# Optimization experiments

Measured on AMD Instinct MI355X. Metric: run time of the kernel, lower is better.

The kernel has to match this reference:

```python
import jax, jax.numpy as jnp
import numpy as np

B, N, M, D = 4, 4096, 4096, 128


def setup_inputs() -> dict:
    key = jax.random.key(0)
    kk, kq, kv = jax.random.split(key, 3)
    return {
        "k": jax.random.normal(kk, (B, N, D), dtype=jnp.float32),
        "q": jax.random.normal(kq, (B, M, D), dtype=jnp.float32),
        "v": jax.random.normal(kv, (B, M, D), dtype=jnp.float32),
    }


def reference(k, q, v):
    # scores: [B, N, M] = k @ q^T
    scores = jnp.einsum("bnd,bmd->bnm", k, q)
    # Original uses nn.Softmax() with no dim; torch's legacy rule resolves
    # dim=0 for 3-D inputs, so softmax is over the batch axis, applied twice.
    w = jax.nn.softmax(jax.nn.softmax(scores, axis=0), axis=0)
    out = jnp.einsum("bnm,bmd->bnd", w, v)
    return out
```

## Files before the change

kernel.cpp:

```cpp
#include <hip/hip_runtime.h>
#include <hip/hip_bf16.h>

#define NB 4
#define NN 4096
#define MM 4096
#define DD 128
#define BN 32
#define BM 64
#define NCH 4
#define OUT_ELEMS ((size_t)NB * NN * DD)

using f32x4  = __attribute__((ext_vector_type(4))) float;
using bf16x8 = __attribute__((ext_vector_type(8))) short;

__device__ __forceinline__ float fast_exp2(float x) {
  return __builtin_amdgcn_exp2f(x);
}

__device__ __forceinline__ int rfl(int x) {
  return __builtin_amdgcn_readfirstlane(x);
}

__device__ __forceinline__ short f2bf(float x) {
  union { __hip_bfloat16 h; short s; } u;
  u.h = __float2bfloat16(x);
  return u.s;
}

__device__ __forceinline__ float bf2f(unsigned short s) {
  union { float f; unsigned u; } u;
  u.u = ((unsigned)s) << 16;
  return u.f;
}

__device__ __forceinline__ bf16x8 pack8(const float* __restrict__ p) {
  float4 a = *(const float4*)p;
  float4 b = *(const float4*)(p + 4);
  bf16x8 r;
  r[0] = f2bf(a.x); r[1] = f2bf(a.y); r[2] = f2bf(a.z); r[3] = f2bf(a.w);
  r[4] = f2bf(b.x); r[5] = f2bf(b.y); r[6] = f2bf(b.z); r[7] = f2bf(b.w);
  return r;
}

__global__ __launch_bounds__(256) void zero_out_kernel(float4* __restrict__ out) {
  out[(size_t)blockIdx.x * 256 + threadIdx.x] = (float4){0.f, 0.f, 0.f, 0.f};
}

__global__ __launch_bounds__(256) void prep_kernel(
    const float* __restrict__ k, const float* __restrict__ q, const float* __restrict__ v,
    unsigned short* __restrict__ kbt, unsigned short* __restrict__ qbt,
    unsigned short* __restrict__ vtt) {
  __shared__ unsigned short t[64][72];
  if (blockIdx.y < 2) {
    const float* src = blockIdx.y ? q : k;
    unsigned short* dst = blockIdx.y ? qbt : kbt;
    const int blk = blockIdx.x;
    const int b = blk >> 8, rf = blk & 255;
    const int kf = threadIdx.x >> 6, l = threadIdx.x & 63;
    const int lr = l & 15, hg = l >> 4;
    const float* s = src + ((size_t)(b * 4096 + rf * 16 + lr) * DD + kf * 32 + hg * 8);
    *(bf16x8*)(dst + (((size_t)((b * 256 + rf) * 4 + kf)) << 9) + (l << 3)) = pack8(s);
    return;
  }
  if (blockIdx.x >= 512) return;
  const int b = blockIdx.x >> 7;
  const int rem = blockIdx.x & 127;
  const int d0 = (rem >> 6) * 64, m0 = (rem & 63) * 64;
  const int r = threadIdx.x >> 2, c4 = threadIdx.x & 3;
  const float* src = v + ((size_t)b * MM + m0 + r) * DD + d0 + c4 * 16;
  for (int j = 0; j < 4; ++j) {
    float4 x = *(const float4*)(src + j * 4);
    int dl = c4 * 16 + j * 4;
    t[dl + 0][r] = (unsigned short)f2bf(x.x);
    t[dl + 1][r] = (unsigned short)f2bf(x.y);
    t[dl + 2][r] = (unsigned short)f2bf(x.z);
    t[dl + 3][r] = (unsigned short)f2bf(x.w);
  }
  __syncthreads();
  const int s8 = threadIdx.x >> 5;
  const int dfl = s8 & 3, mtl = s8 >> 2;
  const int t32 = threadIdx.x & 31;
  for (int ll = 0; ll < 2; ++ll) {
    const int l = t32 * 2 + ll;
    const int lr = l & 15, hg = l >> 4;
    bf16x8 val = *(bf16x8*)&t[dfl * 16 + lr][mtl * 32 + hg * 8];
    *(bf16x8*)(vtt + (((size_t)((b * 8 + (d0 >> 4) + dfl) * 128 + (m0 >> 5) + mtl)) << 9) +
               (l << 3)) = val;
  }
}

__global__ __launch_bounds__(256) void reduce4_frag_kernel(const unsigned short* __restrict__ p,
                                                           float* __restrict__ out) {
  const size_t idx = (size_t)blockIdx.x * 256 + threadIdx.x;
  float r0 = 0.f, r1 = 0.f, r2 = 0.f, r3 = 0.f;
  for (int c = 0; c < NCH; ++c) {
    ushort4 a = *(const ushort4*)(p + (size_t)c * OUT_ELEMS + idx * 4);
    r0 += bf2f(a.x); r1 += bf2f(a.y); r2 += bf2f(a.z); r3 += bf2f(a.w);
  }
  const int l = (int)(idx & 63);
  const int djg = (int)((idx >> 6) & 7);
  const int nf = (int)((idx >> 9) & 255);
  const int bq = (int)(idx >> 17);
  const int lr = l & 15, hg = l >> 4;
  float* o = out + ((size_t)(bq * 4096 + nf * 16 + hg * 4) * DD + djg * 16 + lr);
  o[0] = r0; o[DD] = r1; o[2 * DD] = r2; o[3 * DD] = r3;
}

#define LGKM0_SBAR()                                        \
  do {                                                      \
    asm volatile("s_waitcnt lgkmcnt(0)" ::: "memory");      \
    __builtin_amdgcn_s_barrier();                           \
    asm volatile("" ::: "memory");                          \
  } while (0)

template <bool WS, bool PART>
__global__ __launch_bounds__(512, 4) void attn_fused(
    const float* __restrict__ k, const float* __restrict__ q, const float* __restrict__ v,
    const unsigned short* __restrict__ kbt, const unsigned short* __restrict__ qbt,
    const unsigned short* __restrict__ vtt, void* __restrict__ outp) {
  __shared__ alignas(8)  unsigned short s_pos[NB][8][64][4];
  __shared__ alignas(16) unsigned short Wl[2][NB][BN][BM];

  const int tid = threadIdx.x;
  const int wv = tid >> 6, l = tid & 63, lr = l & 15, hg = l >> 4;
  const int voff = l << 3;
  const int wg = blockIdx.x;
  const int cid = wg & (NCH - 1);
  const int nt = wg >> 2;
  const int n0 = nt * BN;
  const int it0 = cid * (MM / BM / NCH);
  const int it1 = it0 + (MM / BM / NCH);

  const int bq = wv >> 1, h = wv & 1;
  const int h_s = wv >> 2, fi_s = (wv >> 1) & 1, fj_s = wv & 1;

  bf16x8 ka[2][4];
  {
    const unsigned short* kp = WS ? (kbt + rfl(((bq * 256 + nt * 2) * 4) << 9)) : nullptr;
    for (int fn = 0; fn < 2; ++fn)
      for (int kf = 0; kf < 4; ++kf) {
        if (WS) ka[fn][kf] = *(const bf16x8*)(kp + fn * 2048 + kf * 512 + voff);
        else    ka[fn][kf] = pack8(k + ((size_t)bq * NN + n0 + fn * 16 + lr) * DD +
                                   kf * 32 + hg * 8);
      }
  }

  f32x4 acc[2][4];
  for (int fi = 0; fi < 2; ++fi)
    for (int dj = 0; dj < 4; ++dj) acc[fi][dj] = (f32x4){0.f, 0.f, 0.f, 0.f};

  bf16x8 vf[4][2];
  bf16x8 qf[2][4];
  float  p[NB][4];

  auto load_q = [&](int it) {
    if (WS) {
      const unsigned short* qp = qbt + rfl(((bq * 256 + it * 4 + h * 2) * 4) << 9);
      for (int fm = 0; fm < 2; ++fm)
        for (int kf = 0; kf < 4; ++kf)
          qf[fm][kf] = *(const bf16x8*)(qp + fm * 2048 + kf * 512 + voff);
    } else {
      const int m0 = it * BM;
      for (int fm = 0; fm < 2; ++fm)
        for (int kf = 0; kf < 4; ++kf)
          qf[fm][kf] = pack8(q + ((size_t)bq * MM + m0 + h * 32 + fm * 16 + lr) * DD +
                             kf * 32 + hg * 8);
    }
  };

  auto qk_mfma = [&]() {
    f32x4 s[2][2];
    for (int fm = 0; fm < 2; ++fm)
      for (int fn = 0; fn < 2; ++fn) s[fm][fn] = (f32x4){0.f, 0.f, 0.f, 0.f};
    for (int kf = 0; kf < 4; ++kf)
      for (int fm = 0; fm < 2; ++fm)
        for (int fn = 0; fn < 2; ++fn)
          s[fm][fn] = __builtin_amdgcn_mfma_f32_16x16x32_bf16(qf[fm][kf], ka[fn][kf],
                                                              s[fm][fn], 0, 0, 0);
    for (int fm = 0; fm < 2; ++fm)
      for (int fn = 0; fn < 2; ++fn) {
        short4 pk;
        pk.x = f2bf(s[fm][fn][0]); pk.y = f2bf(s[fm][fn][1]);
        pk.z = f2bf(s[fm][fn][2]); pk.w = f2bf(s[fm][fn][3]);
        *(short4*)&s_pos[bq][h * 4 + fm * 2 + fn][l][0] = pk;
      }
  };

  auto issue_v = [&](int it) {
    if (WS) {
      const unsigned short* vp = vtt + rfl((((bq * 8 + h * 4) * 128) + it * 2) << 9);
      for (int dj = 0; dj < 4; ++dj)
        for (int kf = 0; kf < 2; ++kf)
          vf[dj][kf] = *(const bf16x8*)(vp + dj * 65536 + kf * 512 + voff);
    } else {
      const int m0 = it * BM;
      for (int dj = 0; dj < 4; ++dj)
        for (int kf = 0; kf < 2; ++kf) {
          bf16x8 t;
          for (int e = 0; e < 8; ++e)
            t[e] = f2bf(v[((size_t)bq * MM + m0 + kf * 32 + hg * 8 + e) * DD +
                          h * 64 + dj * 16 + lr]);
          vf[dj][kf] = t;
        }
    }
  };

  auto sm_round1 = [&]() {
    const float L2E = 1.4426950408889634f;
    short4 s0 = *(short4*)&s_pos[0][wv][l][0];
    short4 s1 = *(short4*)&s_pos[1][wv][l][0];
    short4 s2 = *(short4*)&s_pos[2][wv][l][0];
    short4 s3 = *(short4*)&s_pos[3][wv][l][0];
    const short* a0 = (const short*)&s0;
    const short* a1 = (const short*)&s1;
    const short* a2 = (const short*)&s2;
    const short* a3 = (const short*)&s3;
    for (int qq = 0; qq < 4; ++qq) {
      float e0 = fast_exp2(bf2f((unsigned short)a0[qq]) * L2E);
      float e1 = fast_exp2(bf2f((unsigned short)a1[qq]) * L2E);
      float e2 = fast_exp2(bf2f((unsigned short)a2[qq]) * L2E);
      float e3 = fast_exp2(bf2f((unsigned short)a3[qq]) * L2E);
      float inv = __builtin_amdgcn_rcpf((e0 + e1) + (e2 + e3)) * L2E;
      p[0][qq] = e0 * inv; p[1][qq] = e1 * inv;
      p[2][qq] = e2 * inv; p[3][qq] = e3 * inv;
    }
  };

  auto sm_round2 = [&](int buf) {
    const int n_loc = fj_s * 16 + lr;
    const int mchunk = (h_s * 4 + fi_s * 2 + (hg >> 1)) ^ (n_loc & 7);
    const int moff = mchunk * 8 + (hg & 1) * 4;
    float w[NB][4];
    for (int qq = 0; qq < 4; ++qq) {
      float f0 = fast_exp2(p[0][qq]), f1 = fast_exp2(p[1][qq]);
      float f2v = fast_exp2(p[2][qq]), f3 = fast_exp2(p[3][qq]);
      float inv2 = __builtin_amdgcn_rcpf((f0 + f1) + (f2v + f3));
      w[0][qq] = f0 * inv2; w[1][qq] = f1 * inv2;
      w[2][qq] = f2v * inv2; w[3][qq] = f3 * inv2;
    }
    for (int bb = 0; bb < NB; ++bb) {
      short4 pk;
      pk.x = f2bf(w[bb][0]); pk.y = f2bf(w[bb][1]);
      pk.z = f2bf(w[bb][2]); pk.w = f2bf(w[bb][3]);
      *(short4*)&Wl[buf][bb][n_loc][moff] = pk;
    }
  };

  auto do_pv = [&](int buf) {
    bf16x8 wf[2][2];
    for (int fi = 0; fi < 2; ++fi)
      for (int kf = 0; kf < 2; ++kf) {
        const int row = fi * 16 + lr, mo = kf * 32 + hg * 8;
        wf[fi][kf] = *(bf16x8*)&Wl[buf][bq][row][mo ^ ((row & 7) << 3)];
      }
    for (int kf = 0; kf < 2; ++kf)
      for (int fi = 0; fi < 2; ++fi)
        for (int dj = 0; dj < 4; ++dj)
          acc[fi][dj] = __builtin_amdgcn_mfma_f32_16x16x32_bf16(wf[fi][kf], vf[dj][kf],
                                                                acc[fi][dj], 0, 0, 0);
  };

  load_q(it0);
  qk_mfma();
  LGKM0_SBAR();
  for (int t = it0; t < it1; ++t) {
    sm_round1();
    LGKM0_SBAR();
    sm_round2(t & 1);
    if (t > it0) do_pv((t - 1) & 1);
    if (t + 1 < it1) {
      load_q(t + 1);
      qk_mfma();
    }
    issue_v(t);
    LGKM0_SBAR();
  }
  do_pv((it1 - 1) & 1);

  if (PART) {
    unsigned short* dst = (unsigned short*)outp + (size_t)cid * OUT_ELEMS +
                          rfl((((bq * 256 + nt * 2) * 8 + h * 4)) << 8);
    for (int fi = 0; fi < 2; ++fi)
      for (int dj = 0; dj < 4; ++dj) {
        short4 pk;
        pk.x = f2bf(acc[fi][dj][0]); pk.y = f2bf(acc[fi][dj][1]);
        pk.z = f2bf(acc[fi][dj][2]); pk.w = f2bf(acc[fi][dj][3]);
        *(short4*)(dst + fi * 2048 + dj * 256 + (l << 2)) = pk;
      }
  } else {
    float* dst = (float*)outp;
    for (int fi = 0; fi < 2; ++fi)
      for (int dj = 0; dj < 4; ++dj)
        for (int qq = 0; qq < 4; ++qq)
          atomicAdd(dst + ((size_t)bq * NN + n0 + fi * 16 + hg * 4 + qq) * DD +
                        h * 64 + dj * 16 + lr,
                    acc[fi][dj][qq]);
  }
}

extern "C" void kernel_launch(void* const* d_in, const int* in_sizes, int n_in,
                              void* d_out, int out_size, void* d_ws, size_t ws_size,
                              hipStream_t stream) {
  (void)in_sizes; (void)n_in; (void)out_size;
  const float* k = (const float*)d_in[0];
  const float* q = (const float*)d_in[1];
  const float* v = (const float*)d_in[2];
  float* out = (float*)d_out;

  const size_t elems = (size_t)NB * MM * DD;
  const size_t need_bf = 3 * elems * sizeof(unsigned short);
  const size_t need_full = need_bf + NCH * OUT_ELEMS * sizeof(unsigned short);
  const bool use_ws = (d_ws != nullptr) && (ws_size >= need_bf);
  const bool use_part = (d_ws != nullptr) && (ws_size >= need_full);

  if (use_ws) {
    unsigned short* kbt = (unsigned short*)d_ws;
    unsigned short* qbt = kbt + elems;
    unsigned short* vtt = qbt + elems;
    prep_kernel<<<dim3(NB * 256, 3), 256, 0, stream>>>(k, q, v, kbt, qbt, vtt);
    if (use_part) {
      unsigned short* partials = vtt + elems;
      attn_fused<true, true><<<dim3(NN / BN * NCH), 512, 0, stream>>>(k, q, v, kbt, qbt, vtt,
                                                                      (void*)partials);
      reduce4_frag_kernel<<<2048, 256, 0, stream>>>(partials, out);
    } else {
      zero_out_kernel<<<(NB * NN * DD) / 4 / 256, 256, 0, stream>>>((float4*)out);
      attn_fused<true, false><<<dim3(NN / BN * NCH), 512, 0, stream>>>(k, q, v, kbt, qbt, vtt,
                                                                       (void*)out);
    }
  } else {
    zero_out_kernel<<<(NB * NN * DD) / 4 / 256, 256, 0, stream>>>((float4*)out);
    attn_fused<false, false><<<dim3(NN / BN * NCH), 512, 0, stream>>>(k, q, v, nullptr,
                                                                      nullptr, nullptr,
                                                                      (void*)out);
  }
}
```

Baseline: 75.01 us.

## Compute per-wave scores across all batches to drop LDS score exchange

Each wave now computes its own 16x16 score tile for all four batches, running the batch-axis double softmax entirely in registers. This removes the shared-memory score buffer and one of the two block barriers per iteration. In exchange, K and Q fragments are reloaded from global memory every iteration for all batches instead of keeping K resident, which raises load traffic. The change also adds MFMA priority hints, a sched_barrier in the barrier macro, and simplifies the V prefetch/PV pipeline ordering.

```diff
diff --git a/kernel.cpp b/kernel.cpp
--- a/kernel.cpp
+++ b/kernel.cpp
@@ -109,8 +109,8 @@
 #define LGKM0_SBAR()                                        \
   do {                                                      \
     asm volatile("s_waitcnt lgkmcnt(0)" ::: "memory");      \
+    __builtin_amdgcn_sched_barrier(0);                      \
     __builtin_amdgcn_s_barrier();                           \
-    asm volatile("" ::: "memory");                          \
   } while (0)
 
 template <bool WS, bool PART>
@@ -118,7 +118,6 @@
     const float* __restrict__ k, const float* __restrict__ q, const float* __restrict__ v,
     const unsigned short* __restrict__ kbt, const unsigned short* __restrict__ qbt,
     const unsigned short* __restrict__ vtt, void* __restrict__ outp) {
-  __shared__ alignas(8)  unsigned short s_pos[NB][8][64][4];
   __shared__ alignas(16) unsigned short Wl[2][NB][BN][BM];
 
   const int tid = threadIdx.x;
@@ -131,60 +130,14 @@
   const int it0 = cid * (MM / BM / NCH);
   const int it1 = it0 + (MM / BM / NCH);
 
+  const int fm = wv >> 1, fn = wv & 1;
   const int bq = wv >> 1, h = wv & 1;
-  const int h_s = wv >> 2, fi_s = (wv >> 1) & 1, fj_s = wv & 1;
-
-  bf16x8 ka[2][4];
-  {
-    const unsigned short* kp = WS ? (kbt + rfl(((bq * 256 + nt * 2) * 4) << 9)) : nullptr;
-    for (int fn = 0; fn < 2; ++fn)
-      for (int kf = 0; kf < 4; ++kf) {
-        if (WS) ka[fn][kf] = *(const bf16x8*)(kp + fn * 2048 + kf * 512 + voff);
-        else    ka[fn][kf] = pack8(k + ((size_t)bq * NN + n0 + fn * 16 + lr) * DD +
-                                   kf * 32 + hg * 8);
-      }
-  }
 
   f32x4 acc[2][4];
   for (int fi = 0; fi < 2; ++fi)
     for (int dj = 0; dj < 4; ++dj) acc[fi][dj] = (f32x4){0.f, 0.f, 0.f, 0.f};
 
   bf16x8 vf[4][2];
-  bf16x8 qf[2][4];
-  float  p[NB][4];
-
-  auto load_q = [&](int it) {
-    if (WS) {
-      const unsigned short* qp = qbt + rfl(((bq * 256 + it * 4 + h * 2) * 4) << 9);
-      for (int fm = 0; fm < 2; ++fm)
-        for (int kf = 0; kf < 4; ++kf)
-          qf[fm][kf] = *(const bf16x8*)(qp + fm * 2048 + kf * 512 + voff);
-    } else {
-      const int m0 = it * BM;
-      for (int fm = 0; fm < 2; ++fm)
-        for (int kf = 0; kf < 4; ++kf)
-          qf[fm][kf] = pack8(q + ((size_t)bq * MM + m0 + h * 32 + fm * 16 + lr) * DD +
-                             kf * 32 + hg * 8);
-    }
-  };
-
-  auto qk_mfma = [&]() {
-    f32x4 s[2][2];
-    for (int fm = 0; fm < 2; ++fm)
-      for (int fn = 0; fn < 2; ++fn) s[fm][fn] = (f32x4){0.f, 0.f, 0.f, 0.f};
-    for (int kf = 0; kf < 4; ++kf)
-      for (int fm = 0; fm < 2; ++fm)
-        for (int fn = 0; fn < 2; ++fn)
-          s[fm][fn] = __builtin_amdgcn_mfma_f32_16x16x32_bf16(qf[fm][kf], ka[fn][kf],
-                                                              s[fm][fn], 0, 0, 0);
-    for (int fm = 0; fm < 2; ++fm)
-      for (int fn = 0; fn < 2; ++fn) {
-        short4 pk;
-        pk.x = f2bf(s[fm][fn][0]); pk.y = f2bf(s[fm][fn][1]);
-        pk.z = f2bf(s[fm][fn][2]); pk.w = f2bf(s[fm][fn][3]);
-        *(short4*)&s_pos[bq][h * 4 + fm * 2 + fn][l][0] = pk;
-      }
-  };
 
   auto issue_v = [&](int it) {
     if (WS) {
@@ -205,44 +158,55 @@
     }
   };
 
-  auto sm_round1 = [&]() {
+  auto qk_sm_write = [&](int t) {
+    const int m0 = t * BM;
+    f32x4 s[NB];
+#pragma unroll
+    for (int b = 0; b < NB; ++b) {
+      bf16x8 kab[4], qfb[4];
+      if (WS) {
+        const unsigned short* kp = kbt + rfl(((b * 256 + nt * 2 + fn) * 4) << 9);
+        const unsigned short* qp = qbt + rfl(((b * 256 + (m0 >> 4) + fm) * 4) << 9);
+        for (int kf = 0; kf < 4; ++kf) {
+          kab[kf] = *(const bf16x8*)(kp + kf * 512 + voff);
+          qfb[kf] = *(const bf16x8*)(qp + kf * 512 + voff);
+        }
+      } else {
+        for (int kf = 0; kf < 4; ++kf) {
+          kab[kf] = pack8(k + ((size_t)b * NN + n0 + fn * 16 + lr) * DD + kf * 32 + hg * 8);
+          qfb[kf] = pack8(q + ((size_t)b * MM + m0 + fm * 16 + lr) * DD + kf * 32 + hg * 8);
+        }
+      }
+      f32x4 sb = (f32x4){0.f, 0.f, 0.f, 0.f};
+      __builtin_amdgcn_s_setprio(1);
+      for (int kf = 0; kf < 4; ++kf)
+        sb = __builtin_amdgcn_mfma_f32_16x16x32_bf16(qfb[kf], kab[kf], sb, 0, 0, 0);
+      __builtin_amdgcn_s_setprio(0);
+      s[b] = sb;
+    }
     const float L2E = 1.4426950408889634f;
-    short4 s0 = *(short4*)&s_pos[0][wv][l][0];
-    short4 s1 = *(short4*)&s_pos[1][wv][l][0];
-    short4 s2 = *(short4*)&s_pos[2][wv][l][0];
-    short4 s3 = *(short4*)&s_pos[3][wv][l][0];
-    const short* a0 = (const short*)&s0;
-    const short* a1 = (const short*)&s1;
-    const short* a2 = (const short*)&s2;
-    const short* a3 = (const short*)&s3;
+    float w[NB][4];
+#pragma unroll
     for (int qq = 0; qq < 4; ++qq) {
-      float e0 = fast_exp2(bf2f((unsigned short)a0[qq]) * L2E);
-      float e1 = fast_exp2(bf2f((unsigned short)a1[qq]) * L2E);
-      float e2 = fast_exp2(bf2f((unsigned short)a2[qq]) * L2E);
-      float e3 = fast_exp2(bf2f((unsigned short)a3[qq]) * L2E);
+      float e0 = fast_exp2(s[0][qq] * L2E), e1 = fast_exp2(s[1][qq] * L2E);
+      float e2 = fast_exp2(s[2][qq] * L2E), e3 = fast_exp2(s[3][qq] * L2E);
       float inv = __builtin_amdgcn_rcpf((e0 + e1) + (e2 + e3)) * L2E;
-      p[0][qq] = e0 * inv; p[1][qq] = e1 * inv;
-      p[2][qq] = e2 * inv; p[3][qq] = e3 * inv;
-    }
-  };
-
-  auto sm_round2 = [&](int buf) {
-    const int n_loc = fj_s * 16 + lr;
-    const int mchunk = (h_s * 4 + fi_s * 2 + (hg >> 1)) ^ (n_loc & 7);
-    const int moff = mchunk * 8 + (hg & 1) * 4;
-    float w[NB][4];
-    for (int qq = 0; qq < 4; ++qq) {
-      float f0 = fast_exp2(p[0][qq]), f1 = fast_exp2(p[1][qq]);
-      float f2v = fast_exp2(p[2][qq]), f3 = fast_exp2(p[3][qq]);
+      float f0 = fast_exp2(e0 * inv), f1 = fast_exp2(e1 * inv);
+      float f2v = fast_exp2(e2 * inv), f3 = fast_exp2(e3 * inv);
       float inv2 = __builtin_amdgcn_rcpf((f0 + f1) + (f2v + f3));
       w[0][qq] = f0 * inv2; w[1][qq] = f1 * inv2;
       w[2][qq] = f2v * inv2; w[3][qq] = f3 * inv2;
     }
-    for (int bb = 0; bb < NB; ++bb) {
+    const int n_loc = fn * 16 + lr;
+    const int mchunk = (fm * 2 + (hg >> 1)) ^ (n_loc & 7);
+    const int moff = mchunk * 8 + (hg & 1) * 4;
+    const int buf = t & 1;
+#pragma unroll
+    for (int b = 0; b < NB; ++b) {
       short4 pk;
-      pk.x = f2bf(w[bb][0]); pk.y = f2bf(w[bb][1]);
-      pk.z = f2bf(w[bb][2]); pk.w = f2bf(w[bb][3]);
-      *(short4*)&Wl[buf][bb][n_loc][moff] = pk;
+      pk.x = f2bf(w[b][0]); pk.y = f2bf(w[b][1]);
+      pk.z = f2bf(w[b][2]); pk.w = f2bf(w[b][3]);
+      *(short4*)&Wl[buf][b][n_loc][moff] = pk;
     }
   };
 
@@ -253,29 +217,22 @@
         const int row = fi * 16 + lr, mo = kf * 32 + hg * 8;
         wf[fi][kf] = *(bf16x8*)&Wl[buf][bq][row][mo ^ ((row & 7) << 3)];
       }
+    __builtin_amdgcn_s_setprio(1);
     for (int kf = 0; kf < 2; ++kf)
       for (int fi = 0; fi < 2; ++fi)
         for (int dj = 0; dj < 4; ++dj)
           acc[fi][dj] = __builtin_amdgcn_mfma_f32_16x16x32_bf16(wf[fi][kf], vf[dj][kf],
                                                                 acc[fi][dj], 0, 0, 0);
+    __builtin_amdgcn_s_setprio(0);
   };
 
-  load_q(it0);
-  qk_mfma();
-  LGKM0_SBAR();
+  issue_v(it0);
   for (int t = it0; t < it1; ++t) {
-    sm_round1();
+    qk_sm_write(t);
     LGKM0_SBAR();
-    sm_round2(t & 1);
-    if (t > it0) do_pv((t - 1) & 1);
-    if (t + 1 < it1) {
-      load_q(t + 1);
-      qk_mfma();
-    }
-    issue_v(t);
-    LGKM0_SBAR();
-  }
-  do_pv((it1 - 1) & 1);
+    do_pv(t & 1);
+    if (t + 1 < it1) issue_v(t + 1);
+  }
 
   if (PART) {
     unsigned short* dst = (unsigned short*)outp + (size_t)cid * OUT_ELEMS +
```

Measured after the change: 108.8 us. +45.0%, slower.
